# Kernel optimization log

Measured on AMD Instinct MI355X. Metric: run time of the kernel, lower is better.

The kernel has to match this reference:

```python
import jax, jax.numpy as jnp
import numpy as np

N_REUPLOADS = 3


def _qrun(x, Wp, bp, W1, b1, W2, b2):
    """Q-RUN layer: linear proj -> sin/cos reupload stack -> tiny per-channel MLP -> flatten.
    x: [..., in_dim]; Wp: [H2, in_dim]; W1: [mlp_h, 2*n_reuploads]; W2: [2, mlp_h].
    Returns [..., 2*H2].
    """
    p = jnp.einsum('...i,hi->...h', x, Wp) + bp                 # [..., H2]
    # features ordered [sin, cos, sin, cos, sin, cos] as in torch.stack of extend-ed list
    sc = jnp.stack([jnp.sin(p), jnp.cos(p)], axis=-1)           # [..., H2, 2]
    feats = jnp.tile(sc, (1,) * (sc.ndim - 1) + (N_REUPLOADS,))  # [..., H2, 6]
    h = jax.nn.relu(jnp.einsum('...k,mk->...m', feats, W1) + b1)  # [..., H2, 32]
    o = jnp.einsum('...m,om->...o', h, W2) + b2                 # [..., H2, 2]
    return o.reshape(o.shape[:-2] + (-1,))                      # flatten(start_dim=-2)


def setup_inputs() -> dict:
    key = jax.random.key(0)
    ks = jax.random.split(key, 20)
    H, I, MH, K = 5120, 27648, 32, 2 * N_REUPLOADS
    d = {}
    d['x'] = jax.random.normal(ks[0], (1, 256, H), dtype=jnp.float32)

    def mk(kbase, in_dim, out_half):
        k1, k2, k3, k4 = jax.random.split(kbase, 4)
        return (
            jax.random.normal(k1, (out_half, in_dim), jnp.float32) * (1.0 / np.sqrt(in_dim)),
            jnp.zeros((out_half,), jnp.float32),
            jax.random.normal(k2, (MH, K), jnp.float32) * 0.1,
            jnp.zeros((MH,), jnp.float32),
            jax.random.normal(k3, (2, MH), jnp.float32) * 0.01,
            jnp.zeros((2,), jnp.float32),
        )

    (d['Wg'], d['bg'], d['W1g'], d['b1g'], d['W2g'], d['b2g']) = mk(ks[1], H, I // 2)
    (d['Wu'], d['bu'], d['W1u'], d['b1u'], d['W2u'], d['b2u']) = mk(ks[2], H, I // 2)
    (d['Wd'], d['bd'], d['W1d'], d['b1d'], d['W2d'], d['b2d']) = mk(ks[3], I, H // 2)
    return d


def reference(x, Wg, bg, W1g, b1g, W2g, b2g,
              Wu, bu, W1u, b1u, W2u, b2u,
              Wd, bd, W1d, b1d, W2d, b2d):
    gate = _qrun(x, Wg, bg, W1g, b1g, W2g, b2g)   # [B,S,27648]
    up = _qrun(x, Wu, bu, W1u, b1u, W2u, b2u)     # [B,S,27648]
    h = jax.nn.silu(gate) * up
    return _qrun(h, Wd, bd, W1d, b1d, W2d, b2d)   # [B,S,5120]
```

## Files before the change

### kernel.cpp

```cpp
#include <hip/hip_runtime.h>
#include <stdint.h>

typedef unsigned short u16;
typedef __attribute__((ext_vector_type(8))) short short8;
typedef __attribute__((ext_vector_type(4))) float f32x4;

#define KGU  5120
#define NPD  2560
#define KD   27648
#define SPLITD 12
#define KCHD 2304
#define PEL (256*2560)

__device__ __forceinline__ uint32_t f2bf(float x) {
  uint32_t b = __float_as_uint(x);
  return (b + 0x7fffu + ((b >> 16) & 1u)) >> 16;
}
__device__ __forceinline__ uint32_t pk2(float lo, float hi) { return f2bf(lo) | (f2bf(hi) << 16); }
__device__ __forceinline__ uint32_t cvtpk(float lo, float hi) {
  uint32_t r;
  asm("v_cvt_pk_bf16_f32 %0, %1, %2" : "=v"(r) : "v"(lo), "v"(hi));
  return r;
}
__device__ __forceinline__ float silu(float x) {
  return x * __builtin_amdgcn_rcpf(1.f + __expf(-x));
}
#define MFMA16(a,b,c) __builtin_amdgcn_mfma_f32_16x16x32_bf16(a, b, c, 0, 0, 0)

__global__ __launch_bounds__(256) void k_cvt(const float* __restrict__ X, u16* __restrict__ XF) {
  const int kt = blockIdx.x;
  const int lane = threadIdx.x & 63, wv = threadIdx.x >> 6;
#pragma unroll
  for (int ii = 0; ii < 4; ++ii) {
    const int mt = wv * 4 + ii;
    const float* src = X + (size_t)(mt * 16 + (lane & 15)) * KGU + kt * 32 + (lane >> 4) * 8;
    float4 f0 = *(const float4*)src;
    float4 f1 = *(const float4*)(src + 4);
    uint4 v;
    v.x = cvtpk(f0.x, f0.y); v.y = cvtpk(f0.z, f0.w);
    v.z = cvtpk(f1.x, f1.y); v.w = cvtpk(f1.z, f1.w);
    *(uint4*)(XF + ((size_t)(kt * 16 + mt) * 64 + lane) * 8) = v;
  }
}

__global__ __launch_bounds__(512, 4)
void k_gu(const u16* __restrict__ XF,
          const float* __restrict__ Wg, const float* __restrict__ bg,
          const float* __restrict__ W1g, const float* __restrict__ b1g,
          const float* __restrict__ W2g, const float* __restrict__ b2g,
          const float* __restrict__ Wu, const float* __restrict__ bu,
          const float* __restrict__ W1u, const float* __restrict__ b1u,
          const float* __restrict__ W2u, const float* __restrict__ b2u,
          u16* __restrict__ HF) {
  __shared__ __align__(16) char smem[66560];
  const int tid = threadIdx.x, lane = tid & 63, wid = tid >> 6;
  const int wm = wid >> 1, wn = wid & 1;
  const int s_ = lane & 15, quad = lane >> 4;
  const int bx = blockIdx.x;
  const int w = (bx & 7) * 54 + (bx >> 3);
  const int j0p = w * 32;

  float4* mc4 = (float4*)(smem + 65536);
  float*  mc1 = (float*)(smem + 65536 + 1024);
  if (tid < 64) {
    int sel = tid >> 5, m = tid & 31;
    const float* w1 = (sel ? W1u : W1g) + m * 6;
    const float* b1 = sel ? b1u : b1g;
    const float* w2 = sel ? W2u : W2g;
    mc4[sel * 32 + m] = make_float4(w1[0] + w1[2] + w1[4], w1[1] + w1[3] + w1[5], b1[m], w2[m]);
    mc1[sel * 32 + m] = w2[32 + m];
  }

  const int kkl = lane >> 3;
  const int s0 = 8 * (wid & 1);
  const int wbase = kkl * 4096 + (wid >> 1) * 1024 + ((lane >> 1) & 3) * 256 + (lane & 1) * 8;
  const float* srcG = Wg + (size_t)(j0p + 4 * wid) * KGU + 4 * lane;
  const float* srcU = Wu + (size_t)(j0p + 4 * wid) * KGU + 4 * lane;

  const int rbase = quad * 256 + (s_ << 4);
  const short8* XFp = (const short8*)XF;

  f32x4 acc[4][2];
#pragma unroll
  for (int i = 0; i < 4; ++i) { acc[i][0] = (f32x4)0.f; acc[i][1] = (f32x4)0.f; }

  float4 sr[8];
#pragma unroll
  for (int i = 0; i < 8; ++i) {
    const float* p = ((i & 1) ? srcU : srcG) + (size_t)(i >> 1) * KGU;
    sr[i] = *(const float4*)p;
  }

#pragma unroll 1
  for (int st = 0; st < 20; ++st) {
    char* buf = smem + (st & 1) * 32768;
#pragma unroll
    for (int i = 0; i < 8; ++i) {
      uint2 v; v.x = cvtpk(sr[i].x, sr[i].y); v.y = cvtpk(sr[i].z, sr[i].w);
      *(uint2*)(buf + wbase + (((s0 + i) ^ kkl) << 4)) = v;
    }
    __builtin_amdgcn_sched_barrier(0);
    if (st < 19) {
      const int kf = (st + 1) * 256;
#pragma unroll
      for (int i = 0; i < 8; ++i) {
        const float* p = ((i & 1) ? srcU : srcG) + (size_t)(i >> 1) * KGU + kf;
        sr[i] = *(const float4*)p;
      }
    }
    __builtin_amdgcn_sched_barrier(0);
    asm volatile("s_waitcnt lgkmcnt(0)" ::: "memory");
    __builtin_amdgcn_s_barrier();
    __builtin_amdgcn_sched_barrier(0);
    const short8* pa = XFp + ((size_t)(st * 8) * 16 + wm * 4) * 64 + lane;
    const char* bb = buf + (wn * 2) * 1024;
#pragma unroll
    for (int kk = 0; kk < 8; ++kk) {
      short8 a0 = pa[(kk * 16 + 0) * 64];
      short8 a1 = pa[(kk * 16 + 1) * 64];
      short8 a2 = pa[(kk * 16 + 2) * 64];
      short8 a3 = pa[(kk * 16 + 3) * 64];
      const int ro = kk * 4096 + (rbase ^ (kk << 4));
      short8 b0 = *(const short8*)(bb + ro);
      short8 b1 = *(const short8*)(bb + ro + 1024);
      __builtin_amdgcn_s_setprio(1);
      acc[0][0] = MFMA16(a0, b0, acc[0][0]); acc[0][1] = MFMA16(a0, b1, acc[0][1]);
      acc[1][0] = MFMA16(a1, b0, acc[1][0]); acc[1][1] = MFMA16(a1, b1, acc[1][1]);
      acc[2][0] = MFMA16(a2, b0, acc[2][0]); acc[2][1] = MFMA16(a2, b1, acc[2][1]);
      acc[3][0] = MFMA16(a3, b0, acc[3][0]); acc[3][1] = MFMA16(a3, b1, acc[3][1]);
      __builtin_amdgcn_s_setprio(0);
    }
  }

  const int sel = lane & 1;
  const float b2v0 = sel ? b2u[0] : b2g[0];
  const float b2v1 = sel ? b2u[1] : b2g[1];
  const float4* mcs = mc4 + sel * 32;
  const float*  mcw = mc1 + sel * 32;
  char* HFb = (char*)HF;
#pragma unroll
  for (int ni = 0; ni < 2; ++ni) {
    const int c = wn * 32 + ni * 16 + s_;
    const int j = j0p + (c >> 1);
    const float bp = sel ? bu[j] : bg[j];
#pragma unroll
    for (int mi = 0; mi < 4; ++mi) {
      float sv[4], cv[4], o0[4], o1[4];
#pragma unroll
      for (int e = 0; e < 4; ++e) {
        float p = acc[mi][ni][e] + bp;
        sv[e] = __sinf(p); cv[e] = __cosf(p);
        o0[e] = b2v0; o1[e] = b2v1;
      }
#pragma unroll 4
      for (int m = 0; m < 32; ++m) {
        float4 k4 = mcs[m]; float w2b = mcw[m];
#pragma unroll
        for (int e = 0; e < 4; ++e) {
          float hh = fmaxf(fmaf(sv[e], k4.x, fmaf(cv[e], k4.y, k4.z)), 0.f);
          o0[e] = fmaf(hh, k4.w, o0[e]);
          o1[e] = fmaf(hh, w2b, o1[e]);
        }
      }
#pragma unroll
      for (int e = 0; e < 4; ++e) {
        float t0 = __shfl_xor(o0[e], 1);
        float t1 = __shfl_xor(o1[e], 1);
        float g0 = sel ? t0 : o0[e];
        float u0 = sel ? o0[e] : t0;
        float g1 = sel ? t1 : o1[e];
        float u1 = sel ? o1[e] : t1;
        float h0 = silu(g0) * u0, h1 = silu(g1) * u1;
        if (!sel) {
          const int row = wm * 64 + mi * 16 + quad * 4 + e;
          const int kt2 = j >> 4, mt2 = wm * 4 + mi;
          const int lf2 = (row & 15) + 16 * ((j >> 2) & 3);
          *(uint32_t*)(HFb + (size_t)(kt2 * 16 + mt2) * 1024 + lf2 * 16 + (j & 3) * 4)
              = pk2(h0, h1);
        }
      }
    }
  }
}

__global__ __launch_bounds__(512, 2)
void k_down(const u16* __restrict__ HF, const float* __restrict__ Wd, float* __restrict__ P2) {
  __shared__ __align__(16) char smem[65536];
  const int tid = threadIdx.x, lane = tid & 63, wid = tid >> 6;
  const int wm = wid >> 1, wn = wid & 1;
  const int s_ = lane & 15, quad = lane >> 4;
  const int bx = blockIdx.x;
  const int w = (bx & 7) * 30 + (bx >> 3);
  const int sk = w / 20, nt = w % 20;
  const int n0 = nt * 128;
  const int kc = sk * KCHD;

  const int b5 = lane >> 5;
  const float* srcD = Wd + (size_t)(n0 + 16 * wid + b5) * KD + kc + 4 * (lane & 31);
  const int kkd = (lane & 31) >> 3;
  const int wbase = kkd * 8192 + wid * 1024 + ((lane & 7) >> 1) * 256 + (lane & 1) * 8;
  const int rbase = quad * 256 + (s_ << 4);
  const short8* HFp = (const short8*)HF;
  const int kc32 = sk * 72;

  f32x4 acc[4][4];
#pragma unroll
  for (int i = 0; i < 4; ++i)
#pragma unroll
    for (int j = 0; j < 4; ++j) acc[i][j] = (f32x4)0.f;

  float4 sr[8];
#pragma unroll
  for (int i = 0; i < 8; ++i) sr[i] = *(const float4*)(srcD + (size_t)(2 * i) * KD);

#pragma unroll 1
  for (int st = 0; st < 18; ++st) {
    char* buf = smem + (st & 1) * 32768;
#pragma unroll
    for (int i = 0; i < 8; ++i) {
      uint2 v; v.x = cvtpk(sr[i].x, sr[i].y); v.y = cvtpk(sr[i].z, sr[i].w);
      *(uint2*)(buf + wbase + (((2 * i + b5) ^ kkd) << 4)) = v;
    }
    __builtin_amdgcn_sched_barrier(0);
    if (st < 17) {
      const int kf = (st + 1) * 128;
#pragma unroll
      for (int i = 0; i < 8; ++i)
        sr[i] = *(const float4*)(srcD + (size_t)(2 * i) * KD + kf);
    }
    __builtin_amdgcn_sched_barrier(0);
    asm volatile("s_waitcnt lgkmcnt(0)" ::: "memory");
    __builtin_amdgcn_s_barrier();
    __builtin_amdgcn_sched_barrier(0);
    const short8* pa = HFp + ((size_t)(kc32 + st * 4) * 16 + wm * 4) * 64 + lane;
    const char* bb = buf + (wn * 4) * 1024;
#pragma unroll
    for (int kk = 0; kk < 4; ++kk) {
      short8 a0 = pa[(kk * 16 + 0) * 64];
      short8 a1 = pa[(kk * 16 + 1) * 64];
      short8 a2 = pa[(kk * 16 + 2) * 64];
      short8 a3 = pa[(kk * 16 + 3) * 64];
      const int ro = kk * 8192 + (rbase ^ (kk << 4));
      short8 b0 = *(const short8*)(bb + ro);
      short8 b1 = *(const short8*)(bb + ro + 1024);
      short8 b2 = *(const short8*)(bb + ro + 2048);
      short8 b3 = *(const short8*)(bb + ro + 3072);
      __builtin_amdgcn_s_setprio(1);
      acc[0][0] = MFMA16(a0, b0, acc[0][0]); acc[0][1] = MFMA16(a0, b1, acc[0][1]);
      acc[0][2] = MFMA16(a0, b2, acc[0][2]); acc[0][3] = MFMA16(a0, b3, acc[0][3]);
      acc[1][0] = MFMA16(a1, b0, acc[1][0]); acc[1][1] = MFMA16(a1, b1, acc[1][1]);
      acc[1][2] = MFMA16(a1, b2, acc[1][2]); acc[1][3] = MFMA16(a1, b3, acc[1][3]);
      acc[2][0] = MFMA16(a2, b0, acc[2][0]); acc[2][1] = MFMA16(a2, b1, acc[2][1]);
      acc[2][2] = MFMA16(a2, b2, acc[2][2]); acc[2][3] = MFMA16(a2, b3, acc[2][3]);
      acc[3][0] = MFMA16(a3, b0, acc[3][0]); acc[3][1] = MFMA16(a3, b1, acc[3][1]);
      acc[3][2] = MFMA16(a3, b2, acc[3][2]); acc[3][3] = MFMA16(a3, b3, acc[3][3]);
      __builtin_amdgcn_s_setprio(0);
    }
  }

  const size_t pb = (size_t)sk * PEL;
#pragma unroll
  for (int mi = 0; mi < 4; ++mi) {
    int mrow = wm * 64 + mi * 16 + (quad << 2);
#pragma unroll
    for (int ni = 0; ni < 4; ++ni) {
      int n = n0 + wn * 64 + ni * 16 + s_;
#pragma unroll
      for (int e = 0; e < 4; ++e)
        P2[pb + (size_t)(mrow + e) * NPD + n] = acc[mi][ni][e];
    }
  }
}

__global__ __launch_bounds__(256) void k_fin(const float* __restrict__ P2, const float* __restrict__ bd,
    const float* __restrict__ W1d, const float* __restrict__ b1d, const float* __restrict__ W2d,
    const float* __restrict__ b2d, float* __restrict__ out) {
  __shared__ float4 mc0[32];
  __shared__ float mc1[32];
  const int tid = threadIdx.x;
  if (tid < 32) {
    const float* w = W1d + tid * 6;
    mc0[tid] = make_float4(w[0] + w[2] + w[4], w[1] + w[3] + w[5], b1d[tid], W2d[tid]);
    mc1[tid] = W2d[32 + tid];
  }
  __syncthreads();
  const int idx = blockIdx.x * 256 + tid;
  const int m = idx / NPD, j = idx - m * NPD;
  float p = bd[j];
#pragma unroll
  for (int sk = 0; sk < SPLITD; ++sk) p += P2[(size_t)sk * PEL + idx];
  float s = __sinf(p), c = __cosf(p);
  float o0 = b2d[0], o1 = b2d[1];
#pragma unroll 4
  for (int mm = 0; mm < 32; ++mm) {
    float4 k = mc0[mm];
    float hh = fmaxf(fmaf(s, k.x, fmaf(c, k.y, k.z)), 0.f);
    o0 = fmaf(hh, k.w, o0);
    o1 = fmaf(hh, mc1[mm], o1);
  }
  *(float2*)&out[(size_t)m * 5120 + 2 * j] = make_float2(o0, o1);
}

extern "C" void kernel_launch(void* const* d_in, const int* in_sizes, int n_in,
                              void* d_out, int out_size, void* d_ws, size_t ws_size,
                              hipStream_t stream) {
  const float* x   = (const float*)d_in[0];
  const float* Wg  = (const float*)d_in[1];
  const float* bg  = (const float*)d_in[2];
  const float* W1g = (const float*)d_in[3];
  const float* b1g = (const float*)d_in[4];
  const float* W2g = (const float*)d_in[5];
  const float* b2g = (const float*)d_in[6];
  const float* Wu  = (const float*)d_in[7];
  const float* bu  = (const float*)d_in[8];
  const float* W1u = (const float*)d_in[9];
  const float* b1u = (const float*)d_in[10];
  const float* W2u = (const float*)d_in[11];
  const float* b2u = (const float*)d_in[12];
  const float* Wd  = (const float*)d_in[13];
  const float* bd  = (const float*)d_in[14];
  const float* W1d = (const float*)d_in[15];
  const float* b1d = (const float*)d_in[16];
  const float* W2d = (const float*)d_in[17];
  const float* b2d = (const float*)d_in[18];
  char* ws = (char*)d_ws;
  u16*  XF = (u16*)ws;
  u16*  HF = (u16*)(ws + 2621440);
  float* P2 = (float*)(ws + 16777216);
  if (ws_size < 48234496u) return;

  k_cvt<<<dim3(160), dim3(256), 0, stream>>>(x, XF);
  k_gu<<<dim3(432), dim3(512), 0, stream>>>(XF, Wg, bg, W1g, b1g, W2g, b2g,
                                            Wu, bu, W1u, b1u, W2u, b2u, HF);
  k_down<<<dim3(240), dim3(512), 0, stream>>>(HF, Wd, P2);
  k_fin<<<dim3(2560), dim3(256), 0, stream>>>(P2, bd, W1d, b1d, W2d, b2d, (float*)d_out);
}
```

Before: 299.6 us.

## Restructure GEMM mainloops with small K-steps, deep register prefetch, smaller LDS tiles

Both the gate/up and down GEMM kernels switch from large 256/128-wide K stages with a 64KB double buffer to 64-wide K steps using a 16KB double-buffered swizzled LDS tile. Weight loads are prefetched four steps ahead in registers, and activation fragments are prefetched one step ahead. The down kernel also halves its N tile to 64, doubles the grid to 480 blocks and raises the occupancy hint to 4. The aim is better latency hiding of the HBM-bound fp32 weight stream through more resident waves and deeper prefetch. The cost is a barrier every small step and less reuse per block.

```diff
diff --git a/kernel.cpp b/kernel.cpp
--- a/kernel.cpp
+++ b/kernel.cpp
@@ -52,7 +52,7 @@
           const float* __restrict__ W1u, const float* __restrict__ b1u,
           const float* __restrict__ W2u, const float* __restrict__ b2u,
           u16* __restrict__ HF) {
-  __shared__ __align__(16) char smem[66560];
+  __shared__ __align__(16) char smem[16384 + 1536];
   const int tid = threadIdx.x, lane = tid & 63, wid = tid >> 6;
   const int wm = wid >> 1, wn = wid & 1;
   const int s_ = lane & 15, quad = lane >> 4;
@@ -60,8 +60,8 @@
   const int w = (bx & 7) * 54 + (bx >> 3);
   const int j0p = w * 32;
 
-  float4* mc4 = (float4*)(smem + 65536);
-  float*  mc1 = (float*)(smem + 65536 + 1024);
+  float4* mc4 = (float4*)(smem + 16384);
+  float*  mc1 = (float*)(smem + 16384 + 1024);
   if (tid < 64) {
     int sel = tid >> 5, m = tid & 31;
     const float* w1 = (sel ? W1u : W1g) + m * 6;
@@ -71,64 +71,74 @@
     mc1[sel * 32 + m] = w2[32 + m];
   }
 
-  const int kkl = lane >> 3;
-  const int s0 = 8 * (wid & 1);
-  const int wbase = kkl * 4096 + (wid >> 1) * 1024 + ((lane >> 1) & 3) * 256 + (lane & 1) * 8;
-  const float* srcG = Wg + (size_t)(j0p + 4 * wid) * KGU + 4 * lane;
-  const float* srcU = Wu + (size_t)(j0p + 4 * wid) * KGU + 4 * lane;
-
-  const int rbase = quad * 256 + (s_ << 4);
+  const int r_loc = 8 * wid + (lane >> 3);
+  const float* srcB = ((r_loc & 1) ? Wu : Wg) + (size_t)(j0p + (r_loc >> 1)) * KGU + (lane & 7) * 8;
+  const int bwr = r_loc * 128 + (((lane & 7) ^ (r_loc & 7)) << 4);
+  const int rb = wn * 32 + s_;
+  const int rsw = s_ & 7;
+
   const short8* XFp = (const short8*)XF;
+  const short8* paB = XFp + ((size_t)wm * 4) * 64 + lane;
 
   f32x4 acc[4][2];
 #pragma unroll
   for (int i = 0; i < 4; ++i) { acc[i][0] = (f32x4)0.f; acc[i][1] = (f32x4)0.f; }
-
-  float4 sr[8];
-#pragma unroll
-  for (int i = 0; i < 8; ++i) {
-    const float* p = ((i & 1) ? srcU : srcG) + (size_t)(i >> 1) * KGU;
-    sr[i] = *(const float4*)p;
-  }
+  float4 sr[4][2];
+  short8 Ag[2][4];
+
+#pragma unroll
+  for (int j = 0; j < 4; ++j) {
+    sr[j][0] = *(const float4*)(srcB + j * 64);
+    sr[j][1] = *(const float4*)(srcB + j * 64 + 4);
+  }
+#pragma unroll
+  for (int kk = 0; kk < 2; ++kk)
+#pragma unroll
+    for (int mi = 0; mi < 4; ++mi) Ag[kk][mi] = paB[(size_t)kk * 1024 + mi * 64];
+  {
+    uint4 v;
+    v.x = cvtpk(sr[0][0].x, sr[0][0].y); v.y = cvtpk(sr[0][0].z, sr[0][0].w);
+    v.z = cvtpk(sr[0][1].x, sr[0][1].y); v.w = cvtpk(sr[0][1].z, sr[0][1].w);
+    *(uint4*)(smem + bwr) = v;
+  }
+  asm volatile("s_waitcnt lgkmcnt(0)" ::: "memory");
+  __builtin_amdgcn_sched_barrier(0);
+  __builtin_amdgcn_s_barrier();
 
 #pragma unroll 1
-  for (int st = 0; st < 20; ++st) {
-    char* buf = smem + (st & 1) * 32768;
-#pragma unroll
-    for (int i = 0; i < 8; ++i) {
-      uint2 v; v.x = cvtpk(sr[i].x, sr[i].y); v.y = cvtpk(sr[i].z, sr[i].w);
-      *(uint2*)(buf + wbase + (((s0 + i) ^ kkl) << 4)) = v;
-    }
-    __builtin_amdgcn_sched_barrier(0);
-    if (st < 19) {
-      const int kf = (st + 1) * 256;
-#pragma unroll
-      for (int i = 0; i < 8; ++i) {
-        const float* p = ((i & 1) ? srcU : srcG) + (size_t)(i >> 1) * KGU + kf;
-        sr[i] = *(const float4*)p;
-      }
-    }
-    __builtin_amdgcn_sched_barrier(0);
-    asm volatile("s_waitcnt lgkmcnt(0)" ::: "memory");
-    __builtin_amdgcn_s_barrier();
-    __builtin_amdgcn_sched_barrier(0);
-    const short8* pa = XFp + ((size_t)(st * 8) * 16 + wm * 4) * 64 + lane;
-    const char* bb = buf + (wn * 2) * 1024;
-#pragma unroll
-    for (int kk = 0; kk < 8; ++kk) {
-      short8 a0 = pa[(kk * 16 + 0) * 64];
-      short8 a1 = pa[(kk * 16 + 1) * 64];
-      short8 a2 = pa[(kk * 16 + 2) * 64];
-      short8 a3 = pa[(kk * 16 + 3) * 64];
-      const int ro = kk * 4096 + (rbase ^ (kk << 4));
-      short8 b0 = *(const short8*)(bb + ro);
-      short8 b1 = *(const short8*)(bb + ro + 1024);
-      __builtin_amdgcn_s_setprio(1);
-      acc[0][0] = MFMA16(a0, b0, acc[0][0]); acc[0][1] = MFMA16(a0, b1, acc[0][1]);
-      acc[1][0] = MFMA16(a1, b0, acc[1][0]); acc[1][1] = MFMA16(a1, b1, acc[1][1]);
-      acc[2][0] = MFMA16(a2, b0, acc[2][0]); acc[2][1] = MFMA16(a2, b1, acc[2][1]);
-      acc[3][0] = MFMA16(a3, b0, acc[3][0]); acc[3][1] = MFMA16(a3, b1, acc[3][1]);
-      __builtin_amdgcn_s_setprio(0);
+  for (int tb = 0; tb < 20; ++tb) {
+#pragma unroll
+    for (int j = 0; j < 4; ++j) {
+      const int st = tb * 4 + j;
+      const char* buf = smem + (j & 1) * 8192;
+#pragma unroll
+      for (int kk = 0; kk < 2; ++kk) {
+        const int so = ((kk * 4 + quad) ^ rsw) << 4;
+        short8 b0 = *(const short8*)(buf + rb * 128 + so);
+        short8 b1 = *(const short8*)(buf + (rb + 16) * 128 + so);
+        __builtin_amdgcn_s_setprio(1);
+        acc[0][0] = MFMA16(Ag[kk][0], b0, acc[0][0]); acc[0][1] = MFMA16(Ag[kk][0], b1, acc[0][1]);
+        acc[1][0] = MFMA16(Ag[kk][1], b0, acc[1][0]); acc[1][1] = MFMA16(Ag[kk][1], b1, acc[1][1]);
+        acc[2][0] = MFMA16(Ag[kk][2], b0, acc[2][0]); acc[2][1] = MFMA16(Ag[kk][2], b1, acc[2][1]);
+        acc[3][0] = MFMA16(Ag[kk][3], b0, acc[3][0]); acc[3][1] = MFMA16(Ag[kk][3], b1, acc[3][1]);
+        __builtin_amdgcn_s_setprio(0);
+        const int stn = (st < 79) ? st + 1 : 79;
+        const short8* pa = paB + (size_t)(stn * 2 + kk) * 1024;
+#pragma unroll
+        for (int mi = 0; mi < 4; ++mi) Ag[kk][mi] = pa[mi * 64];
+      }
+      const int jn = (j + 1) & 3;
+      char* bufn = smem + (((j & 1) ^ 1)) * 8192;
+      uint4 v;
+      v.x = cvtpk(sr[jn][0].x, sr[jn][0].y); v.y = cvtpk(sr[jn][0].z, sr[jn][0].w);
+      v.z = cvtpk(sr[jn][1].x, sr[jn][1].y); v.w = cvtpk(sr[jn][1].z, sr[jn][1].w);
+      *(uint4*)(bufn + bwr) = v;
+      const int stf = (st + 5 < 80) ? st + 5 : 79;
+      sr[jn][0] = *(const float4*)(srcB + stf * 64);
+      sr[jn][1] = *(const float4*)(srcB + stf * 64 + 4);
+      asm volatile("s_waitcnt lgkmcnt(0)" ::: "memory");
+      __builtin_amdgcn_sched_barrier(0);
+      __builtin_amdgcn_s_barrier();
     }
   }
 
@@ -183,91 +193,98 @@
   }
 }
 
-__global__ __launch_bounds__(512, 2)
+__global__ __launch_bounds__(512, 4)
 void k_down(const u16* __restrict__ HF, const float* __restrict__ Wd, float* __restrict__ P2) {
-  __shared__ __align__(16) char smem[65536];
+  __shared__ __align__(16) char smem[16384];
   const int tid = threadIdx.x, lane = tid & 63, wid = tid >> 6;
   const int wm = wid >> 1, wn = wid & 1;
   const int s_ = lane & 15, quad = lane >> 4;
   const int bx = blockIdx.x;
-  const int w = (bx & 7) * 30 + (bx >> 3);
-  const int sk = w / 20, nt = w % 20;
-  const int n0 = nt * 128;
-  const int kc = sk * KCHD;
-
-  const int b5 = lane >> 5;
-  const float* srcD = Wd + (size_t)(n0 + 16 * wid + b5) * KD + kc + 4 * (lane & 31);
-  const int kkd = (lane & 31) >> 3;
-  const int wbase = kkd * 8192 + wid * 1024 + ((lane & 7) >> 1) * 256 + (lane & 1) * 8;
-  const int rbase = quad * 256 + (s_ << 4);
+  const int w = (bx & 7) * 60 + (bx >> 3);
+  const int sk = w / 40, nt = w - sk * 40;
+  const int n0 = nt * 64;
+
+  const int r_loc = 8 * wid + (lane >> 3);
+  const float* srcB = Wd + (size_t)(n0 + r_loc) * KD + sk * KCHD + (lane & 7) * 8;
+  const int bwr = r_loc * 128 + (((lane & 7) ^ (r_loc & 7)) << 4);
+  const int rb = wn * 32 + s_;
+  const int rsw = s_ & 7;
+
   const short8* HFp = (const short8*)HF;
-  const int kc32 = sk * 72;
-
-  f32x4 acc[4][4];
-#pragma unroll
-  for (int i = 0; i < 4; ++i)
-#pragma unroll
-    for (int j = 0; j < 4; ++j) acc[i][j] = (f32x4)0.f;
-
-  float4 sr[8];
-#pragma unroll
-  for (int i = 0; i < 8; ++i) sr[i] = *(const float4*)(srcD + (size_t)(2 * i) * KD);
+  const short8* paB = HFp + ((size_t)(sk * 72) * 16 + wm * 4) * 64 + lane;
+
+  f32x4 acc[4][2];
+#pragma unroll
+  for (int i = 0; i < 4; ++i) { acc[i][0] = (f32x4)0.f; acc[i][1] = (f32x4)0.f; }
+  float4 sr[4][2];
+  short8 Ag[2][4];
+
+#pragma unroll
+  for (int j = 0; j < 4; ++j) {
+    sr[j][0] = *(const float4*)(srcB + j * 64);
+    sr[j][1] = *(const float4*)(srcB + j * 64 + 4);
+  }
+#pragma unroll
+  for (int kk = 0; kk < 2; ++kk)
+#pragma unroll
+    for (int mi = 0; mi < 4; ++mi) Ag[kk][mi] = paB[(size_t)kk * 1024 + mi * 64];
+  {
+    uint4 v;
+    v.x = cvtpk(sr[0][0].x, sr[0][0].y); v.y = cvtpk(sr[0][0].z, sr[0][0].w);
+    v.z = cvtpk(sr[0][1].x, sr[0][1].y); v.w = cvtpk(sr[0][1].z, sr[0][1].w);
+    *(uint4*)(smem + bwr) = v;
+  }
+  asm volatile("s_waitcnt lgkmcnt(0)" ::: "memory");
+  __builtin_amdgcn_sched_barrier(0);
+  __builtin_amdgcn_s_barrier();
 
 #pragma unroll 1
-  for (int st = 0; st < 18; ++st) {
-    char* buf = smem + (st & 1) * 32768;
-#pragma unroll
-    for (int i = 0; i < 8; ++i) {
-      uint2 v; v.x = cvtpk(sr[i].x, sr[i].y); v.y = cvtpk(sr[i].z, sr[i].w);
-      *(uint2*)(buf + wbase + (((2 * i + b5) ^ kkd) << 4)) = v;
+  for (int tb = 0; tb < 9; ++tb) {
+#pragma unroll
+    for (int j = 0; j < 4; ++j) {
+      const int st = tb * 4 + j;
+      const char* buf = smem + (j & 1) * 8192;
+#pragma unroll
+      for (int kk = 0; kk < 2; ++kk) {
+        const int so = ((kk * 4 + quad) ^ rsw) << 4;
+        short8 b0 = *(const short8*)(buf + rb * 128 + so);
+        short8 b1 = *(const short8*)(buf + (rb + 16) * 128 + so);
+        __builtin_amdgcn_s_setprio(1);
+        acc[0][0] = MFMA16(Ag[kk][0], b0, acc[0][0]); acc[0][1] = MFMA16(Ag[kk][0], b1, acc[0][1]);
+        acc[1][0] = MFMA16(Ag[kk][1], b0, acc[1][0]); acc[1][1] = MFMA16(Ag[kk][1], b1, acc[1][1]);
+        acc[2][0] = MFMA16(Ag[kk][2], b0, acc[2][0]); acc[2][1] = MFMA16(Ag[kk][2], b1, acc[2][1]);
+        acc[3][0] = MFMA16(Ag[kk][3], b0, acc[3][0]); acc[3][1] = MFMA16(Ag[kk][3], b1, acc[3][1]);
+        __builtin_amdgcn_s_setprio(0);
+        const int stn = (st < 35) ? st + 1 : 35;
+        const short8* pa = paB + (size_t)(stn * 2 + kk) * 1024;
+#pragma unroll
+        for (int mi = 0; mi < 4; ++mi) Ag[kk][mi] = pa[mi * 64];
+      }
+      const int jn = (j + 1) & 3;
+      char* bufn = smem + (((j & 1) ^ 1)) * 8192;
+      uint4 v;
+      v.x = cvtpk(sr[jn][0].x, sr[jn][0].y); v.y = cvtpk(sr[jn][0].z, sr[jn][0].w);
+      v.z = cvtpk(sr[jn][1].x, sr[jn][1].y); v.w = cvtpk(sr[jn][1].z, sr[jn][1].w);
+      *(uint4*)(bufn + bwr) = v;
+      const int stf = (st + 5 < 36) ? st + 5 : 35;
+      sr[jn][0] = *(const float4*)(srcB + stf * 64);
+      sr[jn][1] = *(const float4*)(srcB + stf * 64 + 4);
+      asm volatile("s_waitcnt lgkmcnt(0)" ::: "memory");
+      __builtin_amdgcn_sched_barrier(0);
+      __builtin_amdgcn_s_barrier();
     }
-    __builtin_amdgcn_sched_barrier(0);
-    if (st < 17) {
-      const int kf = (st + 1) * 128;
-#pragma unroll
-      for (int i = 0; i < 8; ++i)
-        sr[i] = *(const float4*)(srcD + (size_t)(2 * i) * KD + kf);
-    }
-    __builtin_amdgcn_sched_barrier(0);
-    asm volatile("s_waitcnt lgkmcnt(0)" ::: "memory");
-    __builtin_amdgcn_s_barrier();
-    __builtin_amdgcn_sched_barrier(0);
-    const short8* pa = HFp + ((size_t)(kc32 + st * 4) * 16 + wm * 4) * 64 + lane;
-    const char* bb = buf + (wn * 4) * 1024;
-#pragma unroll
-    for (int kk = 0; kk < 4; ++kk) {
-      short8 a0 = pa[(kk * 16 + 0) * 64];
-      short8 a1 = pa[(kk * 16 + 1) * 64];
-      short8 a2 = pa[(kk * 16 + 2) * 64];
-      short8 a3 = pa[(kk * 16 + 3) * 64];
-      const int ro = kk * 8192 + (rbase ^ (kk << 4));
-      short8 b0 = *(const short8*)(bb + ro);
-      short8 b1 = *(const short8*)(bb + ro + 1024);
-      short8 b2 = *(const short8*)(bb + ro + 2048);
-      short8 b3 = *(const short8*)(bb + ro + 3072);
-      __builtin_amdgcn_s_setprio(1);
-      acc[0][0] = MFMA16(a0, b0, acc[0][0]); acc[0][1] = MFMA16(a0, b1, acc[0][1]);
-      acc[0][2] = MFMA16(a0, b2, acc[0][2]); acc[0][3] = MFMA16(a0, b3, acc[0][3]);
-      acc[1][0] = MFMA16(a1, b0, acc[1][0]); acc[1][1] = MFMA16(a1, b1, acc[1][1]);
-      acc[1][2] = MFMA16(a1, b2, acc[1][2]); acc[1][3] = MFMA16(a1, b3, acc[1][3]);
-      acc[2][0] = MFMA16(a2, b0, acc[2][0]); acc[2][1] = MFMA16(a2, b1, acc[2][1]);
-      acc[2][2] = MFMA16(a2, b2, acc[2][2]); acc[2][3] = MFMA16(a2, b3, acc[2][3]);
-      acc[3][0] = MFMA16(a3, b0, acc[3][0]); acc[3][1] = MFMA16(a3, b1, acc[3][1]);
-      acc[3][2] = MFMA16(a3, b2, acc[3][2]); acc[3][3] = MFMA16(a3, b3, acc[3][3]);
-      __builtin_amdgcn_s_setprio(0);
-    }
-  }
-
-  const size_t pb = (size_t)sk * PEL;
+  }
+
+  float* P = P2 + (size_t)sk * PEL;
 #pragma unroll
   for (int mi = 0; mi < 4; ++mi) {
     int mrow = wm * 64 + mi * 16 + (quad << 2);
 #pragma unroll
-    for (int ni = 0; ni < 4; ++ni) {
-      int n = n0 + wn * 64 + ni * 16 + s_;
+    for (int ni = 0; ni < 2; ++ni) {
+      int n = n0 + wn * 32 + ni * 16 + s_;
 #pragma unroll
       for (int e = 0; e < 4; ++e)
-        P2[pb + (size_t)(mrow + e) * NPD + n] = acc[mi][ni][e];
+        P[(size_t)(mrow + e) * NPD + n] = acc[mi][ni][e];
     }
   }
 }
@@ -332,6 +349,6 @@
   k_cvt<<<dim3(160), dim3(256), 0, stream>>>(x, XF);
   k_gu<<<dim3(432), dim3(512), 0, stream>>>(XF, Wg, bg, W1g, b1g, W2g, b2g,
                                             Wu, bu, W1u, b1u, W2u, b2u, HF);
-  k_down<<<dim3(240), dim3(512), 0, stream>>>(HF, Wd, P2);
+  k_down<<<dim3(480), dim3(512), 0, stream>>>(HF, Wd, P2);
   k_fin<<<dim3(2560), dim3(256), 0, stream>>>(P2, bd, W1d, b1d, W2d, b2d, (float*)d_out);
 }
```

New measurement: 315.8 us. 5.4% more time.

## Drop LDS staging in GEMM kernels; load fp32 weights straight into MFMA registers

Applied to the files above, without the earlier changes.

Both the gate/up and down GEMM kernels stop staging weight tiles through shared memory. Each lane now loads its own fp32 weight fragment directly from global memory, converts it to bf16 in registers, and feeds it to MFMA using a two-stage register double buffer. Blocks shrink to 256 threads with a 64-wide N tile per block, and the down kernel doubles its grid to 480 blocks. This removes LDS writes, reads and barriers, but global weight loads become less coalesced (8 floats per lane spread across rows) and register pressure rises.

```diff
diff --git a/kernel.cpp b/kernel.cpp
--- a/kernel.cpp
+++ b/kernel.cpp
@@ -43,7 +43,7 @@
   }
 }
 
-__global__ __launch_bounds__(512, 4)
+__global__ __launch_bounds__(256)
 void k_gu(const u16* __restrict__ XF,
           const float* __restrict__ Wg, const float* __restrict__ bg,
           const float* __restrict__ W1g, const float* __restrict__ b1g,
@@ -52,104 +52,105 @@
           const float* __restrict__ W1u, const float* __restrict__ b1u,
           const float* __restrict__ W2u, const float* __restrict__ b2u,
           u16* __restrict__ HF) {
-  __shared__ __align__(16) char smem[66560];
-  const int tid = threadIdx.x, lane = tid & 63, wid = tid >> 6;
-  const int wm = wid >> 1, wn = wid & 1;
+  __shared__ float4 mc4[64];
+  __shared__ float  mc1s[64];
+  const int tid = threadIdx.x, lane = tid & 63, wv = tid >> 6;
   const int s_ = lane & 15, quad = lane >> 4;
-  const int bx = blockIdx.x;
-  const int w = (bx & 7) * 54 + (bx >> 3);
-  const int j0p = w * 32;
-
-  float4* mc4 = (float4*)(smem + 65536);
-  float*  mc1 = (float*)(smem + 65536 + 1024);
+  const int j0p = blockIdx.x * 32;
+
   if (tid < 64) {
     int sel = tid >> 5, m = tid & 31;
     const float* w1 = (sel ? W1u : W1g) + m * 6;
     const float* b1 = sel ? b1u : b1g;
     const float* w2 = sel ? W2u : W2g;
     mc4[sel * 32 + m] = make_float4(w1[0] + w1[2] + w1[4], w1[1] + w1[3] + w1[5], b1[m], w2[m]);
-    mc1[sel * 32 + m] = w2[32 + m];
-  }
-
-  const int kkl = lane >> 3;
-  const int s0 = 8 * (wid & 1);
-  const int wbase = kkl * 4096 + (wid >> 1) * 1024 + ((lane >> 1) & 3) * 256 + (lane & 1) * 8;
-  const float* srcG = Wg + (size_t)(j0p + 4 * wid) * KGU + 4 * lane;
-  const float* srcU = Wu + (size_t)(j0p + 4 * wid) * KGU + 4 * lane;
-
-  const int rbase = quad * 256 + (s_ << 4);
-  const short8* XFp = (const short8*)XF;
-
-  f32x4 acc[4][2];
-#pragma unroll
-  for (int i = 0; i < 4; ++i) { acc[i][0] = (f32x4)0.f; acc[i][1] = (f32x4)0.f; }
-
-  float4 sr[8];
-#pragma unroll
-  for (int i = 0; i < 8; ++i) {
-    const float* p = ((i & 1) ? srcU : srcG) + (size_t)(i >> 1) * KGU;
-    sr[i] = *(const float4*)p;
-  }
-
+    mc1s[sel * 32 + m] = w2[32 + m];
+  }
+  __syncthreads();
+
+  const short8* pa = (const short8*)XF + ((size_t)wv * 4) * 64 + lane;
+  const float* pb[4];
+#pragma unroll
+  for (int ni = 0; ni < 4; ++ni) {
+    const int c = ni * 16 + s_;
+    pb[ni] = ((c & 1) ? Wu : Wg) + (size_t)(j0p + (c >> 1)) * KGU + quad * 8;
+  }
+
+  f32x4 acc[4][4];
+#pragma unroll
+  for (int i = 0; i < 4; ++i)
+#pragma unroll
+    for (int j = 0; j < 4; ++j) acc[i][j] = (f32x4)0.f;
+
+  short8 A0[4], A1[4];
+  float4 B0[4][2], B1[4][2];
+
+  auto LA = [&](short8* A, int kt) {
+#pragma unroll
+    for (int mi = 0; mi < 4; ++mi) A[mi] = pa[((size_t)kt * 16 + mi) * 64];
+  };
+  auto LB = [&](float4 (*B)[2], int kt) {
+#pragma unroll
+    for (int ni = 0; ni < 4; ++ni) {
+      B[ni][0] = *(const float4*)(pb[ni] + kt * 32);
+      B[ni][1] = *(const float4*)(pb[ni] + kt * 32 + 4);
+    }
+  };
+  auto CV = [&](float4 (*B)[2], short8* bf) {
+#pragma unroll
+    for (int ni = 0; ni < 4; ++ni) {
+      union { uint32_t u[4]; short8 s; } cv;
+      cv.u[0] = cvtpk(B[ni][0].x, B[ni][0].y);
+      cv.u[1] = cvtpk(B[ni][0].z, B[ni][0].w);
+      cv.u[2] = cvtpk(B[ni][1].x, B[ni][1].y);
+      cv.u[3] = cvtpk(B[ni][1].z, B[ni][1].w);
+      bf[ni] = cv.s;
+    }
+  };
+  auto MM = [&](short8* A, short8* bf) {
+    __builtin_amdgcn_s_setprio(1);
+#pragma unroll
+    for (int mi = 0; mi < 4; ++mi)
+#pragma unroll
+      for (int ni = 0; ni < 4; ++ni)
+        acc[mi][ni] = MFMA16(A[mi], bf[ni], acc[mi][ni]);
+    __builtin_amdgcn_s_setprio(0);
+  };
+
+  LB(B0, 0); LA(A0, 0); LB(B1, 1); LA(A1, 1);
 #pragma unroll 1
-  for (int st = 0; st < 20; ++st) {
-    char* buf = smem + (st & 1) * 32768;
-#pragma unroll
-    for (int i = 0; i < 8; ++i) {
-      uint2 v; v.x = cvtpk(sr[i].x, sr[i].y); v.y = cvtpk(sr[i].z, sr[i].w);
-      *(uint2*)(buf + wbase + (((s0 + i) ^ kkl) << 4)) = v;
-    }
-    __builtin_amdgcn_sched_barrier(0);
-    if (st < 19) {
-      const int kf = (st + 1) * 256;
-#pragma unroll
-      for (int i = 0; i < 8; ++i) {
-        const float* p = ((i & 1) ? srcU : srcG) + (size_t)(i >> 1) * KGU + kf;
-        sr[i] = *(const float4*)p;
-      }
-    }
-    __builtin_amdgcn_sched_barrier(0);
-    asm volatile("s_waitcnt lgkmcnt(0)" ::: "memory");
-    __builtin_amdgcn_s_barrier();
-    __builtin_amdgcn_sched_barrier(0);
-    const short8* pa = XFp + ((size_t)(st * 8) * 16 + wm * 4) * 64 + lane;
-    const char* bb = buf + (wn * 2) * 1024;
-#pragma unroll
-    for (int kk = 0; kk < 8; ++kk) {
-      short8 a0 = pa[(kk * 16 + 0) * 64];
-      short8 a1 = pa[(kk * 16 + 1) * 64];
-      short8 a2 = pa[(kk * 16 + 2) * 64];
-      short8 a3 = pa[(kk * 16 + 3) * 64];
-      const int ro = kk * 4096 + (rbase ^ (kk << 4));
-      short8 b0 = *(const short8*)(bb + ro);
-      short8 b1 = *(const short8*)(bb + ro + 1024);
-      __builtin_amdgcn_s_setprio(1);
-      acc[0][0] = MFMA16(a0, b0, acc[0][0]); acc[0][1] = MFMA16(a0, b1, acc[0][1]);
-      acc[1][0] = MFMA16(a1, b0, acc[1][0]); acc[1][1] = MFMA16(a1, b1, acc[1][1]);
-      acc[2][0] = MFMA16(a2, b0, acc[2][0]); acc[2][1] = MFMA16(a2, b1, acc[2][1]);
-      acc[3][0] = MFMA16(a3, b0, acc[3][0]); acc[3][1] = MFMA16(a3, b1, acc[3][1]);
-      __builtin_amdgcn_s_setprio(0);
-    }
+  for (int t = 0; t < 80; ++t) {
+    int k2 = 2 * t + 2; if (k2 > 159) k2 = 159;
+    int k3 = 2 * t + 3; if (k3 > 159) k3 = 159;
+    short8 bf[4];
+    CV(B0, bf);
+    LB(B0, k2);
+    MM(A0, bf);
+    LA(A0, k2);
+    CV(B1, bf);
+    LB(B1, k3);
+    MM(A1, bf);
+    LA(A1, k3);
   }
 
   const int sel = lane & 1;
   const float b2v0 = sel ? b2u[0] : b2g[0];
   const float b2v1 = sel ? b2u[1] : b2g[1];
   const float4* mcs = mc4 + sel * 32;
-  const float*  mcw = mc1 + sel * 32;
+  const float*  mcw = mc1s + sel * 32;
   char* HFb = (char*)HF;
 #pragma unroll
-  for (int ni = 0; ni < 2; ++ni) {
-    const int c = wn * 32 + ni * 16 + s_;
+  for (int ni = 0; ni < 4; ++ni) {
+    const int c = ni * 16 + s_;
     const int j = j0p + (c >> 1);
     const float bp = sel ? bu[j] : bg[j];
 #pragma unroll
     for (int mi = 0; mi < 4; ++mi) {
-      float sv[4], cv[4], o0[4], o1[4];
+      float sv[4], cvv[4], o0[4], o1[4];
 #pragma unroll
       for (int e = 0; e < 4; ++e) {
         float p = acc[mi][ni][e] + bp;
-        sv[e] = __sinf(p); cv[e] = __cosf(p);
+        sv[e] = __sinf(p); cvv[e] = __cosf(p);
         o0[e] = b2v0; o1[e] = b2v1;
       }
 #pragma unroll 4
@@ -157,7 +158,7 @@
         float4 k4 = mcs[m]; float w2b = mcw[m];
 #pragma unroll
         for (int e = 0; e < 4; ++e) {
-          float hh = fmaxf(fmaf(sv[e], k4.x, fmaf(cv[e], k4.y, k4.z)), 0.f);
+          float hh = fmaxf(fmaf(sv[e], k4.x, fmaf(cvv[e], k4.y, k4.z)), 0.f);
           o0[e] = fmaf(hh, k4.w, o0[e]);
           o1[e] = fmaf(hh, w2b, o1[e]);
         }
@@ -172,10 +173,11 @@
         float u1 = sel ? o1[e] : t1;
         float h0 = silu(g0) * u0, h1 = silu(g1) * u1;
         if (!sel) {
-          const int row = wm * 64 + mi * 16 + quad * 4 + e;
-          const int kt2 = j >> 4, mt2 = wm * 4 + mi;
+          const int row = wv * 64 + mi * 16 + quad * 4 + e;
+          const int mt2 = wv * 4 + mi;
+          const int kt2 = j >> 4;
           const int lf2 = (row & 15) + 16 * ((j >> 2) & 3);
-          *(uint32_t*)(HFb + (size_t)(kt2 * 16 + mt2) * 1024 + lf2 * 16 + (j & 3) * 4)
+          *(uint32_t*)(HFb + ((size_t)(kt2 * 16 + mt2) * 64 + lf2) * 16 + (j & 3) * 4)
               = pk2(h0, h1);
         }
       }
@@ -183,25 +185,22 @@
   }
 }
 
-__global__ __launch_bounds__(512, 2)
+__global__ __launch_bounds__(256)
 void k_down(const u16* __restrict__ HF, const float* __restrict__ Wd, float* __restrict__ P2) {
-  __shared__ __align__(16) char smem[65536];
-  const int tid = threadIdx.x, lane = tid & 63, wid = tid >> 6;
-  const int wm = wid >> 1, wn = wid & 1;
+  const int tid = threadIdx.x, lane = tid & 63, wv = tid >> 6;
   const int s_ = lane & 15, quad = lane >> 4;
   const int bx = blockIdx.x;
-  const int w = (bx & 7) * 30 + (bx >> 3);
-  const int sk = w / 20, nt = w % 20;
-  const int n0 = nt * 128;
-  const int kc = sk * KCHD;
-
-  const int b5 = lane >> 5;
-  const float* srcD = Wd + (size_t)(n0 + 16 * wid + b5) * KD + kc + 4 * (lane & 31);
-  const int kkd = (lane & 31) >> 3;
-  const int wbase = kkd * 8192 + wid * 1024 + ((lane & 7) >> 1) * 256 + (lane & 1) * 8;
-  const int rbase = quad * 256 + (s_ << 4);
-  const short8* HFp = (const short8*)HF;
-  const int kc32 = sk * 72;
+  const int w = (bx & 7) * 60 + (bx >> 3);
+  const int sk = w / 40, nt = w - sk * 40;
+  const int n0 = nt * 64;
+
+  const short8* pa = (const short8*)HF + ((size_t)(sk * 72) * 16 + wv * 4) * 64 + lane;
+  const float* pb[4];
+#pragma unroll
+  for (int ni = 0; ni < 4; ++ni) {
+    const int c = ni * 16 + s_;
+    pb[ni] = Wd + (size_t)(n0 + c) * KD + sk * KCHD + quad * 8;
+  }
 
   f32x4 acc[4][4];
 #pragma unroll
@@ -209,65 +208,67 @@
 #pragma unroll
     for (int j = 0; j < 4; ++j) acc[i][j] = (f32x4)0.f;
 
-  float4 sr[8];
-#pragma unroll
-  for (int i = 0; i < 8; ++i) sr[i] = *(const float4*)(srcD + (size_t)(2 * i) * KD);
-
+  short8 A0[4], A1[4];
+  float4 B0[4][2], B1[4][2];
+
+  auto LA = [&](short8* A, int kt) {
+#pragma unroll
+    for (int mi = 0; mi < 4; ++mi) A[mi] = pa[((size_t)kt * 16 + mi) * 64];
+  };
+  auto LB = [&](float4 (*B)[2], int kt) {
+#pragma unroll
+    for (int ni = 0; ni < 4; ++ni) {
+      B[ni][0] = *(const float4*)(pb[ni] + kt * 32);
+      B[ni][1] = *(const float4*)(pb[ni] + kt * 32 + 4);
+    }
+  };
+  auto CV = [&](float4 (*B)[2], short8* bf) {
+#pragma unroll
+    for (int ni = 0; ni < 4; ++ni) {
+      union { uint32_t u[4]; short8 s; } cv;
+      cv.u[0] = cvtpk(B[ni][0].x, B[ni][0].y);
+      cv.u[1] = cvtpk(B[ni][0].z, B[ni][0].w);
+      cv.u[2] = cvtpk(B[ni][1].x, B[ni][1].y);
+      cv.u[3] = cvtpk(B[ni][1].z, B[ni][1].w);
+      bf[ni] = cv.s;
+    }
+  };
+  auto MM = [&](short8* A, short8* bf) {
+    __builtin_amdgcn_s_setprio(1);
+#pragma unroll
+    for (int mi = 0; mi < 4; ++mi)
+#pragma unroll
+      for (int ni = 0; ni < 4; ++ni)
+        acc[mi][ni] = MFMA16(A[mi], bf[ni], acc[mi][ni]);
+    __builtin_amdgcn_s_setprio(0);
+  };
+
+  LB(B0, 0); LA(A0, 0); LB(B1, 1); LA(A1, 1);
 #pragma unroll 1
-  for (int st = 0; st < 18; ++st) {
-    char* buf = smem + (st & 1) * 32768;
-#pragma unroll
-    for (int i = 0; i < 8; ++i) {
-      uint2 v; v.x = cvtpk(sr[i].x, sr[i].y); v.y = cvtpk(sr[i].z, sr[i].w);
-      *(uint2*)(buf + wbase + (((2 * i + b5) ^ kkd) << 4)) = v;
-    }
-    __builtin_amdgcn_sched_barrier(0);
-    if (st < 17) {
-      const int kf = (st + 1) * 128;
-#pragma unroll
-      for (int i = 0; i < 8; ++i)
-        sr[i] = *(const float4*)(srcD + (size_t)(2 * i) * KD + kf);
-    }
-    __builtin_amdgcn_sched_barrier(0);
-    asm volatile("s_waitcnt lgkmcnt(0)" ::: "memory");
-    __builtin_amdgcn_s_barrier();
-    __builtin_amdgcn_sched_barrier(0);
-    const short8* pa = HFp + ((size_t)(kc32 + st * 4) * 16 + wm * 4) * 64 + lane;
-    const char* bb = buf + (wn * 4) * 1024;
-#pragma unroll
-    for (int kk = 0; kk < 4; ++kk) {
-      short8 a0 = pa[(kk * 16 + 0) * 64];
-      short8 a1 = pa[(kk * 16 + 1) * 64];
-      short8 a2 = pa[(kk * 16 + 2) * 64];
-      short8 a3 = pa[(kk * 16 + 3) * 64];
-      const int ro = kk * 8192 + (rbase ^ (kk << 4));
-      short8 b0 = *(const short8*)(bb + ro);
-      short8 b1 = *(const short8*)(bb + ro + 1024);
-      short8 b2 = *(const short8*)(bb + ro + 2048);
-      short8 b3 = *(const short8*)(bb + ro + 3072);
-      __builtin_amdgcn_s_setprio(1);
-      acc[0][0] = MFMA16(a0, b0, acc[0][0]); acc[0][1] = MFMA16(a0, b1, acc[0][1]);
-      acc[0][2] = MFMA16(a0, b2, acc[0][2]); acc[0][3] = MFMA16(a0, b3, acc[0][3]);
-      acc[1][0] = MFMA16(a1, b0, acc[1][0]); acc[1][1] = MFMA16(a1, b1, acc[1][1]);
-      acc[1][2] = MFMA16(a1, b2, acc[1][2]); acc[1][3] = MFMA16(a1, b3, acc[1][3]);
-      acc[2][0] = MFMA16(a2, b0, acc[2][0]); acc[2][1] = MFMA16(a2, b1, acc[2][1]);
-      acc[2][2] = MFMA16(a2, b2, acc[2][2]); acc[2][3] = MFMA16(a2, b3, acc[2][3]);
-      acc[3][0] = MFMA16(a3, b0, acc[3][0]); acc[3][1] = MFMA16(a3, b1, acc[3][1]);
-      acc[3][2] = MFMA16(a3, b2, acc[3][2]); acc[3][3] = MFMA16(a3, b3, acc[3][3]);
-      __builtin_amdgcn_s_setprio(0);
-    }
-  }
-
-  const size_t pb = (size_t)sk * PEL;
+  for (int t = 0; t < 36; ++t) {
+    int k2 = 2 * t + 2; if (k2 > 71) k2 = 71;
+    int k3 = 2 * t + 3; if (k3 > 71) k3 = 71;
+    short8 bf[4];
+    CV(B0, bf);
+    LB(B0, k2);
+    MM(A0, bf);
+    LA(A0, k2);
+    CV(B1, bf);
+    LB(B1, k3);
+    MM(A1, bf);
+    LA(A1, k3);
+  }
+
+  float* P = P2 + (size_t)sk * PEL;
 #pragma unroll
   for (int mi = 0; mi < 4; ++mi) {
-    int mrow = wm * 64 + mi * 16 + (quad << 2);
-#pragma unroll
-    for (int ni = 0; ni < 4; ++ni) {
-      int n = n0 + wn * 64 + ni * 16 + s_;
+    const int row = wv * 64 + mi * 16 + (quad << 2);
+#pragma unroll
+    for (int ni = 0; ni < 4; ++ni) {
+      const int n = n0 + ni * 16 + s_;
 #pragma unroll
       for (int e = 0; e < 4; ++e)
-        P2[pb + (size_t)(mrow + e) * NPD + n] = acc[mi][ni][e];
+        P[(size_t)(row + e) * NPD + n] = acc[mi][ni][e];
     }
   }
 }
@@ -330,8 +331,8 @@
   if (ws_size < 48234496u) return;
 
   k_cvt<<<dim3(160), dim3(256), 0, stream>>>(x, XF);
-  k_gu<<<dim3(432), dim3(512), 0, stream>>>(XF, Wg, bg, W1g, b1g, W2g, b2g,
+  k_gu<<<dim3(432), dim3(256), 0, stream>>>(XF, Wg, bg, W1g, b1g, W2g, b2g,
                                             Wu, bu, W1u, b1u, W2u, b2u, HF);
-  k_down<<<dim3(240), dim3(512), 0, stream>>>(HF, Wd, P2);
+  k_down<<<dim3(480), dim3(256), 0, stream>>>(HF, Wd, P2);
   k_fin<<<dim3(2560), dim3(256), 0, stream>>>(P2, bd, W1d, b1d, W2d, b2d, (float*)d_out);
 }
```

Measured after the change: 582.6 us. +94.5%, slower.
